# Performance work log

Measured on AMD Instinct MI355X. Metric: run time of the kernel, lower is better.

Reference implementation:

```python
import jax, jax.numpy as jnp
import numpy as np

B = 64        # number of tasks (sequential steps)
D = 512       # knowledge_representation_dim == understanding_representation_dim
M = 8192      # memory_slots
GAMMA = 0.95  # memory_gamma


def setup_inputs() -> dict:
    key = jax.random.key(0)
    k1, k2, k3, k4 = jax.random.split(key, 4)
    ortho = jax.nn.initializers.orthogonal()
    return {
        "k": jax.random.normal(k1, (B, 1, D), jnp.float32),
        "u": jax.random.normal(k2, (B, 1, D), jnp.float32),
        "memory_knowledge": ortho(k3, (D, M), jnp.float32),
        "memory_understanding": ortho(k4, (D, M), jnp.float32),
        "beta_param": jnp.float32(0.0),
        "memory_gamma": jnp.float32(GAMMA),
    }


def reference(k, u, memory_knowledge, memory_understanding, beta_param, memory_gamma):
    n_slots = memory_knowledge.shape[1]
    slot_ids = jnp.arange(n_slots)
    beta = jax.nn.sigmoid(beta_param)

    def step(carry, xs):
        MK, MU, w_w, w_u, w_lu = carry
        k_task, u_task = xs  # each [1, D]
        # cosine similarity of the task key against every memory column: [1, M]
        sim = (k_task @ MK) / (
            jnp.linalg.norm(k_task, axis=-1, keepdims=True)
            * jnp.linalg.norm(MK, axis=0, keepdims=True)
        )
        w_r = jax.nn.softmax(sim, axis=-1)[0]  # [M]
        # zero out the least-used slot (argmin of usage weights)
        keep = (slot_ids != jnp.argmin(w_u))[None, :]  # [1, M]
        MK = jnp.where(keep, MK, 0.0)
        MU = jnp.where(keep, MU, 0.0)
        # usage / write / least-used weight updates
        w_u = memory_gamma * w_u + w_r + w_w
        w_w = beta * jnp.mean(w_r) + (1.0 - beta) * w_lu  # [M] via broadcast of scalar mean
        w_lu = (slot_ids == jnp.argmin(w_u)).astype(MK.dtype)  # one-hot least-used
        # rank-1 write of understanding, then read refined understanding, then write knowledge
        MU = MU + u_task[0][:, None] * w_w[None, :]  # [D, M]
        u_ref = w_r @ MK.T  # [D] -- read uses MK after zeroing, before its write
        MK = MK + k_task[0][:, None] * w_w[None, :]  # [D, M]
        return (MK, MU, w_w, w_u, w_lu), u_ref

    zeros = jnp.zeros((n_slots,), memory_knowledge.dtype)
    init = (memory_knowledge, memory_understanding, zeros, zeros, zeros)
    _, u_refined = jax.lax.scan(step, init, (k, u))
    return u_refined[:, None, :]  # [B, 1, D]
```

## Files before the change

kernel.cpp:

```cpp
#include <hip/hip_runtime.h>
#include <math.h>

#define BB 64
#define DD 512
#define MM 8192
#define K2T 512
#define K2C 16

typedef unsigned long long u64;

template<int CTRL>
__device__ __forceinline__ float dpp_addf(float x) {
    int y = __builtin_amdgcn_update_dpp(0, __float_as_int(x), CTRL, 0xF, 0xF, true);
    return x + __int_as_float(y);
}
__device__ __forceinline__ float wave_sum64(float x) {
    x = dpp_addf<0x111>(x); x = dpp_addf<0x112>(x); x = dpp_addf<0x114>(x); x = dpp_addf<0x118>(x);
    x = dpp_addf<0x142>(x); x = dpp_addf<0x143>(x);
    return __int_as_float(__builtin_amdgcn_readlane(__float_as_int(x), 63));
}
template<int CTRL>
__device__ __forceinline__ u64 dpp_min_step(u64 k) {
    unsigned lo = (unsigned)k, hi = (unsigned)(k >> 32);
    unsigned nlo = (unsigned)__builtin_amdgcn_update_dpp((int)0xFFFFFFFFu, (int)lo, CTRL, 0xF, 0xF, false);
    unsigned nhi = (unsigned)__builtin_amdgcn_update_dpp((int)0xFFFFFFFFu, (int)hi, CTRL, 0xF, 0xF, false);
    u64 nk = (((u64)nhi) << 32) | (u64)nlo;
    return nk < k ? nk : k;
}
__device__ __forceinline__ u64 wave_min64(u64 k) {
    k = dpp_min_step<0x111>(k); k = dpp_min_step<0x112>(k); k = dpp_min_step<0x114>(k);
    k = dpp_min_step<0x118>(k); k = dpp_min_step<0x142>(k); k = dpp_min_step<0x143>(k);
    unsigned lo = (unsigned)__builtin_amdgcn_readlane((int)(unsigned)k, 63);
    unsigned hi = (unsigned)__builtin_amdgcn_readlane((int)(unsigned)(k >> 32), 63);
    return (((u64)hi) << 32) | (u64)lo;
}
__device__ __forceinline__ u64 wave_min8(u64 k) {
    k = dpp_min_step<0x111>(k); k = dpp_min_step<0x112>(k); k = dpp_min_step<0x114>(k);
    unsigned lo = (unsigned)__builtin_amdgcn_readlane((int)(unsigned)k, 7);
    unsigned hi = (unsigned)__builtin_amdgcn_readlane((int)(unsigned)(k >> 32), 7);
    return (((u64)hi) << 32) | (u64)lo;
}
__device__ __forceinline__ float readlane_f(float v, int l) {
    return __int_as_float(__builtin_amdgcn_readlane(__float_as_int(v), l));
}

__global__ __launch_bounds__(1024) void k0_gram(const float* __restrict__ K, float* __restrict__ G,
                                                float* __restrict__ Pfx) {
    __shared__ float Ks[BB][129];
    __shared__ float Gs[BB][BB];
    int tid = threadIdx.x;
    int s = tid & 63, tq = tid >> 6;
    float acc[4] = {0.f, 0.f, 0.f, 0.f};
    for (int d0 = 0; d0 < DD; d0 += 128) {
        #pragma unroll
        for (int i = 0; i < 8; ++i) {
            int e = i * 1024 + tid; int r = e >> 7, c = e & 127;
            Ks[r][c] = K[r * DD + d0 + c];
        }
        __syncthreads();
        for (int dl = 0; dl < 128; ++dl) {
            float kv = Ks[s][dl];
            #pragma unroll
            for (int i = 0; i < 4; ++i) acc[i] += Ks[tq * 4 + i][dl] * kv;
        }
        __syncthreads();
    }
    #pragma unroll
    for (int i = 0; i < 4; ++i) {
        G[(tq * 4 + i) * BB + s] = acc[i];
        Gs[tq * 4 + i][s] = acc[i];
    }
    __syncthreads();
    #pragma unroll
    for (int r = 0; r < 4; ++r) {
        int row = tq * 4 + r;
        float x = (s < row) ? Gs[row][s] : 0.f;
        #pragma unroll
        for (int o = 1; o < 64; o <<= 1) {
            float y = __shfl_down(x, o);
            if (s + o < 64) x += y;
        }
        Pfx[row * BB + s] = x;
    }
}

__global__ __launch_bounds__(256) void k1_s0(const float* __restrict__ K, const float* __restrict__ MK0,
                                             float* __restrict__ S0p, float* __restrict__ n2p) {
    __shared__ float Ks[64 * 65];
    __shared__ float Ms[64 * 65];
    __shared__ float sq[4 * 64];
    const int tid = threadIdx.x;
    const int lane = tid & 63, w = tid >> 6;
    const int jb = blockIdx.x * 64;
    const int dbase = blockIdx.y * 256;
    const int t4 = ((w << 2) | (lane >> 4)) << 2;
    const int jq0 = lane & 15;
    float acc[4][4];
    #pragma unroll
    for (int i = 0; i < 4; ++i)
        #pragma unroll
        for (int q = 0; q < 4; ++q) acc[i][q] = 0.f;
    float sqa = 0.f;
    for (int dt = 0; dt < 4; ++dt) {
        int d0 = dbase + dt * 64;
        #pragma unroll
        for (int i = 0; i < 16; ++i) {
            int e = i * 256 + tid; int r = e >> 6, c = e & 63;
            Ks[r * 65 + c] = K[r * DD + d0 + c];
            float m = MK0[(d0 + r) * MM + jb + c];
            Ms[r * 65 + c] = m;
            sqa += m * m;
        }
        __syncthreads();
        #pragma unroll 4
        for (int dl = 0; dl < 64; ++dl) {
            float kv[4], mv[4];
            #pragma unroll
            for (int i = 0; i < 4; ++i) kv[i] = Ks[(t4 + i) * 65 + dl];
            #pragma unroll
            for (int q = 0; q < 4; ++q) mv[q] = Ms[dl * 65 + jq0 + 16 * q];
            #pragma unroll
            for (int i = 0; i < 4; ++i)
                #pragma unroll
                for (int q = 0; q < 4; ++q) acc[i][q] += kv[i] * mv[q];
        }
        __syncthreads();
    }
    #pragma unroll
    for (int i = 0; i < 4; ++i)
        #pragma unroll
        for (int q = 0; q < 4; ++q)
            S0p[blockIdx.y * BB * MM + (t4 + i) * MM + jb + jq0 + 16 * q] = acc[i][q];
    sq[w * 64 + lane] = sqa;
    __syncthreads();
    if (w == 0) n2p[blockIdx.y * MM + jb + lane] =
        sq[lane] + sq[64 + lane] + sq[128 + lane] + sq[192 + lane];
}

__global__ __launch_bounds__(256) void k1b_ecold(const float* __restrict__ S0p,
                                                 const float* __restrict__ G,
                                                 const float* __restrict__ Pfx,
                                                 const float* __restrict__ n2p,
                                                 const float* __restrict__ bp,
                                                 float* __restrict__ Ecold) {
    __shared__ float Pfx0s[BB], invks[BB], k2s[BB];
    int tid = threadIdx.x;
    int j = blockIdx.x * 256 + tid;
    if (tid < BB) {
        float g = G[tid * BB + tid];
        k2s[tid] = g;
        invks[tid] = __builtin_amdgcn_rsqf(g);
        Pfx0s[tid] = Pfx[tid * BB + 0];
    }
    const float beta = 1.f / (1.f + expf(-bp[0]));
    const float cuni = beta / (float)MM;
    float n2c = n2p[j] + n2p[MM + j];
    __syncthreads();
    for (int t = 0; t < BB; ++t) {
        float s0 = S0p[t * MM + j] + S0p[(BB + t) * MM + j];
        float d_ = s0 + cuni * Pfx0s[t];
        float cosv = d_ * invks[t] * __builtin_amdgcn_rsqf(n2c);
        float ee = __expf(cosv);
        Ecold[t * MM + j] = ee;
        n2c = n2c + 2.f * cuni * d_ + cuni * cuni * k2s[t];
    }
}

__global__ __launch_bounds__(256) void ks_rowsum(const float* __restrict__ Ecold, float* __restrict__ Scold) {
    __shared__ float sw[4];
    int t = blockIdx.x, tid = threadIdx.x;
    int lane = tid & 63, wid = tid >> 6;
    float s = 0.f;
    #pragma unroll
    for (int i = 0; i < 32; ++i) s += Ecold[t * MM + i * 256 + tid];
    #pragma unroll
    for (int o = 32; o > 0; o >>= 1) s += __shfl_down(s, o);
    if (lane == 0) sw[wid] = s;
    __syncthreads();
    if (tid == 0) Scold[t] = sw[0] + sw[1] + sw[2] + sw[3];
}

struct ScanSmem {
    u64   red[2][8];
    float EtabL[BB * BB];
    float EcTabL[BB * BB];
    float invSL[BB];
    float SL[BB];
    int   endL[BB];
};
struct K3Smem {
    float Ws[64 * 65];
    float Msub[64 * 65];
};
#define SMEM_BYTES ((sizeof(ScanSmem) > sizeof(K3Smem)) ? sizeof(ScanSmem) : sizeof(K3Smem))

__global__ __launch_bounds__(512) void k23_scan_u1(const float* __restrict__ Ecold,
                                                   const float* __restrict__ G,
                                                   const float* __restrict__ Pfx,
                                                   const float* __restrict__ Scoldg,
                                                   const float* __restrict__ bp,
                                                   const float* __restrict__ gp,
                                                   const float* __restrict__ MK0,
                                                   float* __restrict__ Etab_g,
                                                   float* __restrict__ EcTab_g,
                                                   float* __restrict__ Sg,
                                                   float* __restrict__ invSg,
                                                   int*   __restrict__ endTab_g,
                                                   int*   __restrict__ hcolg,
                                                   float* __restrict__ parts) {
    __shared__ __align__(16) char smem_raw[SMEM_BYTES];
    const int tid = threadIdx.x;

    if (blockIdx.x != 0) {
        K3Smem* sm = (K3Smem*)smem_raw;
        const int tile = blockIdx.x - 1;
        const int d0 = (tile & 7) * 64;
        const int by = tile >> 3;
        const bool act = tid < 256;
        const int lane = tid & 63, w = tid >> 6;
        const int t4 = ((w << 2) | (lane >> 4)) << 2;
        const int dq0 = lane & 15;
        float acc[4][4];
        #pragma unroll
        for (int i = 0; i < 4; ++i)
            #pragma unroll
            for (int q = 0; q < 4; ++q) acc[i][q] = 0.f;
        for (int sub = 0; sub < 4; ++sub) {
            int jb = by * 256 + sub * 64;
            if (act) {
                #pragma unroll
                for (int i = 0; i < 16; ++i) {
                    int e = i * 256 + tid; int r = e >> 6, c = e & 63;
                    sm->Ws[r * 65 + c] = Ecold[r * MM + jb + c];
                    sm->Msub[r * 65 + c] = MK0[(d0 + r) * MM + jb + c];
                }
            }
            __syncthreads();
            if (act) {
                #pragma unroll 4
                for (int jl = 0; jl < 64; ++jl) {
                    float wv[4], mv[4];
                    #pragma unroll
                    for (int i = 0; i < 4; ++i) wv[i] = sm->Ws[(t4 + i) * 65 + jl];
                    #pragma unroll
                    for (int q = 0; q < 4; ++q) mv[q] = sm->Msub[(dq0 + 16 * q) * 65 + jl];
                    #pragma unroll
                    for (int i = 0; i < 4; ++i)
                        #pragma unroll
                        for (int q = 0; q < 4; ++q) acc[i][q] += wv[i] * mv[q];
                }
            }
            __syncthreads();
        }
        if (act) {
            #pragma unroll
            for (int i = 0; i < 4; ++i)
                #pragma unroll
                for (int q = 0; q < 4; ++q)
                    parts[(by * 64 + t4 + i) * DD + d0 + dq0 + 16 * q] = acc[i][q];
        }
        return;
    }

    ScanSmem* sm = (ScanSmem*)smem_raw;
    const int lane = tid & 63;
    const int wid = tid >> 6;

    const float beta  = 1.f / (1.f + expf(-bp[0]));
    const float gamma = gp[0];
    const float cuni  = beta / (float)MM;
    const float omb   = 1.f - beta;

    if (tid < BB) sm->endL[tid] = BB;

    const float4* Ec4 = reinterpret_cast<const float4*>(Ecold);

    float wu[K2C], eb0[K2C], eb1[K2C];
    #pragma unroll
    for (int c = 0; c < K2C; ++c) wu[c] = 0.f;
    #pragma unroll
    for (int i = 0; i < K2C / 4; ++i) {
        float4 v = Ec4[i * K2T + tid];
        eb0[4 * i + 0] = v.x; eb0[4 * i + 1] = v.y; eb0[4 * i + 2] = v.z; eb0[4 * i + 3] = v.w;
    }

    float slot_n2 = 0.f, slot_E = 0.f, slot_ec = 0.f, slot_ecpf = 0.f, wu_hot = 0.f;
    int   slot_j = -1;
    bool  slot_act = false;

    float grow_c = G[lane], pfx_c = Pfx[lane];
    float Ssc_c = Scoldg[0];
    __syncthreads();

    auto step = [&](int t, float (&cur)[K2C], float (&nxt)[K2C]) {
        int j0; float minval;
        if (t == 0) { j0 = 0; minval = 0.f; }
        else {
            u64 pm = sm->red[t & 1][lane & 7];
            pm = wave_min8(pm);
            j0 = (int)(pm & 0xFFFFFFFFu);
            minval = __uint_as_float((unsigned)(pm >> 32));
        }

        float latev = 0.f;
        if (lane == t) latev = Ecold[t * MM + j0];
        if (t + 1 < BB) {
            int js = (lane == t) ? j0 : slot_j;
            if (slot_act || lane == t) slot_ecpf = Ecold[(t + 1) * MM + js];
        }
        float grow_n = (t + 1 < BB) ? G[(t + 1) * BB + lane] : 0.f;
        float pfx_n  = (t + 1 < BB) ? Pfx[(t + 1) * BB + lane] : 0.f;
        float Ssc_n  = (t + 1 < BB) ? Scoldg[t + 1] : 0.f;
        __builtin_amdgcn_sched_barrier(0);
        if (t + 1 < BB) {
            #pragma unroll
            for (int i = 0; i < K2C / 4; ++i) {
                float4 v = Ec4[(t + 1) * (MM / 4) + i * K2T + tid];
                nxt[4 * i + 0] = v.x; nxt[4 * i + 1] = v.y; nxt[4 * i + 2] = v.z; nxt[4 * i + 3] = v.w;
            }
        }
        __builtin_amdgcn_sched_barrier(0);

        const float k2t  = readlane_f(grow_c, t);
        const float invk = __builtin_amdgcn_rsqf(k2t);

        u64 sup = __ballot(slot_act && (slot_j == j0));
        const bool has_sup = (sup != 0ull);
        const int  ssup = has_sup ? (int)__builtin_ctzll(sup) : 0;

        float myDelta = 0.f, e_true = 0.f;
        if (slot_act) {
            float d_ = cuni * pfx_c;
            if (lane >= 1) d_ += omb * grow_c;
            e_true = __expf(d_ * invk * __builtin_amdgcn_rsqf(slot_n2));
            myDelta = e_true - slot_ec;
            slot_E = e_true;
            slot_n2 = slot_n2 + 2.f * cuni * d_ + cuni * cuni * k2t;
        }

        const float S = Ssc_c + wave_sum64(myDelta);
        const float invS = __builtin_amdgcn_rcpf(S);
        const float cuni_t = (t == 0) ? 0.f : cuni;

        if (slot_act) {
            float ww = cuni + ((t >= 2 && lane == t - 1) ? omb : 0.f);
            wu_hot = fmaf(gamma, wu_hot, fmaf(e_true, invS, ww));
        }

        float trans_wu = readlane_f(wu_hot, ssup);
        float trans_E  = readlane_f(e_true, ssup);
        if (lane == t) {
            slot_j = j0;
            float ww0 = cuni + ((t >= 1) ? omb : 0.f);
            slot_n2 = ww0 * ww0 * k2t;
            slot_act = true;
            slot_ec = latev;
            float fresh_wu = fmaf(gamma, minval, fmaf(latev, invS, cuni_t));
            wu_hot = has_sup ? trans_wu : fresh_wu;
            slot_E = has_sup ? trans_E : latev;
        }
        if (has_sup) {
            if (lane == ssup) slot_act = false;
            if (wid == 0 && lane == t) sm->endL[ssup] = t;
        }

        float vmin = 0.f; int jmin = 0;
        #pragma unroll
        for (int i = 0; i < 4; ++i) {
            #pragma unroll
            for (int q = 0; q < 4; ++q) {
                int c = i * 4 + q;
                float wun = fmaf(gamma, wu[c], fmaf(cur[c], invS, cuni_t));
                wu[c] = wun;
                int j = i * 2048 + (tid << 2) + q;
                if (c == 0) { vmin = wun; jmin = j; }
                else if (wun < vmin) { vmin = wun; jmin = j; }
            }
        }
        u64 key = (((u64)__float_as_uint(vmin)) << 32) | (unsigned)jmin;

        if (((j0 >> 2) & (K2T - 1)) == tid) {
            int cj = ((j0 >> 11) << 2) | (j0 & 3);
            #pragma unroll
            for (int c = 0; c < K2C; ++c) if (c == cj) wu[c] = __builtin_inff();
        }

        u64 skey = slot_act ? ((((u64)__float_as_uint(wu_hot)) << 32) | (unsigned)slot_j) : ~0ull;
        key = skey < key ? skey : key;
        key = wave_min64(key);
        if (lane == 0) sm->red[(t + 1) & 1][wid] = key;

        if (wid == 0) {
            sm->EtabL[t * BB + lane]  = slot_E;
            sm->EcTabL[t * BB + lane] = slot_ec;
            if (lane == 0) { sm->invSL[t] = invS; sm->SL[t] = S; }
        }

        if (slot_act) slot_ec = slot_ecpf;
        grow_c = grow_n; pfx_c = pfx_n; Ssc_c = Ssc_n;

        asm volatile("s_waitcnt lgkmcnt(0)" ::: "memory");
        __builtin_amdgcn_s_barrier();
        asm volatile("" ::: "memory");
    };

    #pragma unroll 1
    for (int th = 0; th < BB; th += 2) {
        step(th, eb0, eb1);
        step(th + 1, eb1, eb0);
    }

    for (int i = tid; i < BB * BB; i += K2T) {
        Etab_g[i]  = sm->EtabL[i];
        EcTab_g[i] = sm->EcTabL[i];
    }
    if (tid < BB) {
        Sg[tid] = sm->SL[tid];
        invSg[tid] = sm->invSL[tid];
        endTab_g[tid] = sm->endL[tid];
    }
    if (wid == 0) hcolg[lane] = slot_j;
}

__global__ __launch_bounds__(512) void k3b_gather(const float* __restrict__ MK0, const int* __restrict__ hcolg,
                                                  float* __restrict__ MKhot) {
    int i = blockIdx.x, d = threadIdx.x;
    int h = hcolg[i];
    MKhot[i * DD + d] = MK0[d * MM + h];
}

__global__ __launch_bounds__(512) void k4_final(const float* __restrict__ parts,
                                                const float* __restrict__ K,
                                                const float* __restrict__ Etab,
                                                const float* __restrict__ EcTab,
                                                const int*   __restrict__ endTab,
                                                const float* __restrict__ Sg,
                                                const float* __restrict__ invSg,
                                                const float* __restrict__ MKhot,
                                                const float* __restrict__ bp,
                                                float* __restrict__ out) {
    __shared__ float Arow[BB];
    __shared__ float Drow[BB];
    int t = blockIdx.x, d = threadIdx.x;
    if (d < BB) {
        const float beta = 1.f / (1.f + expf(-bp[0]));
        const float cuni = beta / (float)MM;
        const float omb  = 1.f - beta;
        int s = d;
        float Ev = Etab[t * BB + s];
        int endv = endTab[s];
        bool act = (s <= t) && (t < endv);
        float S = Sg[t], invS = invSg[t];
        float ev = act ? Ev : 0.f;
        float x = ev;
        #pragma unroll
        for (int o = 1; o < 64; o <<= 1) {
            float y = __shfl_down(x, o);
            if (s + o < 64) x += y;
        }
        float suf = x - ev;
        float arow = 0.f;
        if (s < t) {
            float Qe = S - suf;
            arow = cuni * Qe;
            if (s >= 1 && act) arow += omb * Ev;
            arow *= invS;
        }
        Arow[s] = arow;
        Drow[s] = act ? (-invS * EcTab[t * BB + s]) : 0.f;
    }
    __syncthreads();
    float isv = invSg[t];
    float s1 = 0.f;
    #pragma unroll
    for (int p = 0; p < 32; ++p) s1 += parts[(p * 64 + t) * DD + d];
    float s2 = 0.f;
    for (int i = 0; i < BB; ++i) s2 += Drow[i] * MKhot[i * DD + d];
    float s3 = 0.f;
    for (int i = 0; i < BB; ++i) s3 += Arow[i] * K[i * DD + d];
    out[t * DD + d] = isv * s1 + s2 + s3;
}

extern "C" void kernel_launch(void* const* d_in, const int* in_sizes, int n_in,
                              void* d_out, int out_size, void* d_ws, size_t ws_size,
                              hipStream_t stream) {
    const float* K   = (const float*)d_in[0];
    const float* MK0 = (const float*)d_in[2];
    const float* bp  = (const float*)d_in[4];
    const float* gp  = (const float*)d_in[5];

    float* ws    = (float*)d_ws;
    float* G     = ws;
    float* Pfx   = G + 4096;
    float* S0p   = Pfx + 4096;
    float* n2p   = S0p + 1048576;
    float* Ecold = n2p + 16384;
    float* Scold = Ecold + 524288;
    float* Etab  = Scold + 64;
    float* EcTab = Etab + 4096;
    float* Sarr  = EcTab + 4096;
    float* invS  = Sarr + 64;
    float* MKhot = invS + 64;
    float* parts = MKhot + 32768;
    int*   hcol  = (int*)(parts + 1048576);
    int*   endT  = hcol + 64;
    float* out   = (float*)d_out;

    k0_gram     <<<1, 1024, 0, stream>>>(K, G, Pfx);
    k1_s0       <<<dim3(128, 2), 256, 0, stream>>>(K, MK0, S0p, n2p);
    k1b_ecold   <<<32, 256, 0, stream>>>(S0p, G, Pfx, n2p, bp, Ecold);
    ks_rowsum   <<<64, 256, 0, stream>>>(Ecold, Scold);
    k23_scan_u1 <<<257, 512, 0, stream>>>(Ecold, G, Pfx, Scold, bp, gp, MK0,
                                          Etab, EcTab, Sarr, invS, endT, hcol, parts);
    k3b_gather  <<<64, 512, 0, stream>>>(MK0, hcol, MKhot);
    k4_final    <<<64, 512, 0, stream>>>(parts, K, Etab, EcTab, endT, Sarr, invS, MKhot, bp, out);
}
```

Before: 253.6 us.

## Merge gram and S0 kernels; restrict scan slot logic to wave zero

Folds the single-block Gram/prefix kernel into the S0 GEMM kernel as an extra block 0, which removes one launch and lets the two run concurrently. In the sequential scan, the hot-slot bookkeeping now runs only on wave 0, and invS reaches the other waves through shared memory behind an added barrier. Fresh-slot initialisation moves after the key reduction, and the wave min reads lane 63 directly instead of using readlanes. This adds a second barrier per scan step, which may offset the savings on the serial critical path.

```diff
diff --git a/kernel.cpp b/kernel.cpp
--- a/kernel.cpp
+++ b/kernel.cpp
@@ -27,12 +27,10 @@
     u64 nk = (((u64)nhi) << 32) | (u64)nlo;
     return nk < k ? nk : k;
 }
-__device__ __forceinline__ u64 wave_min64(u64 k) {
+__device__ __forceinline__ u64 wave_min64_lane63(u64 k) {
     k = dpp_min_step<0x111>(k); k = dpp_min_step<0x112>(k); k = dpp_min_step<0x114>(k);
     k = dpp_min_step<0x118>(k); k = dpp_min_step<0x142>(k); k = dpp_min_step<0x143>(k);
-    unsigned lo = (unsigned)__builtin_amdgcn_readlane((int)(unsigned)k, 63);
-    unsigned hi = (unsigned)__builtin_amdgcn_readlane((int)(unsigned)(k >> 32), 63);
-    return (((u64)hi) << 32) | (u64)lo;
+    return k;
 }
 __device__ __forceinline__ u64 wave_min8(u64 k) {
     k = dpp_min_step<0x111>(k); k = dpp_min_step<0x112>(k); k = dpp_min_step<0x114>(k);
@@ -44,55 +42,80 @@
     return __int_as_float(__builtin_amdgcn_readlane(__float_as_int(v), l));
 }
 
-__global__ __launch_bounds__(1024) void k0_gram(const float* __restrict__ K, float* __restrict__ G,
-                                                float* __restrict__ Pfx) {
-    __shared__ float Ks[BB][129];
-    __shared__ float Gs[BB][BB];
-    int tid = threadIdx.x;
-    int s = tid & 63, tq = tid >> 6;
-    float acc[4] = {0.f, 0.f, 0.f, 0.f};
-    for (int d0 = 0; d0 < DD; d0 += 128) {
-        #pragma unroll
-        for (int i = 0; i < 8; ++i) {
-            int e = i * 1024 + tid; int r = e >> 7, c = e & 127;
-            Ks[r][c] = K[r * DD + d0 + c];
-        }
+struct K0Smem {
+    float Ks[BB][129];
+    float Gs[BB][BB];
+};
+struct K1Smem {
+    float Ks[64 * 65];
+    float Ms[64 * 65];
+    float sq[4 * 64];
+};
+#define KA_SMEM ((sizeof(K0Smem) > sizeof(K1Smem)) ? sizeof(K0Smem) : sizeof(K1Smem))
+
+__global__ __launch_bounds__(256) void ka_gram_s0(const float* __restrict__ K, const float* __restrict__ MK0,
+                                                  float* __restrict__ G, float* __restrict__ Pfx,
+                                                  float* __restrict__ S0p, float* __restrict__ n2p) {
+    __shared__ __align__(16) char blob[KA_SMEM];
+    const int tid = threadIdx.x;
+
+    if (blockIdx.x == 0) {
+        K0Smem* sm = (K0Smem*)blob;
+        const int ti = ((tid >> 4) & 15) << 2;
+        const int tj = (tid & 15) << 2;
+        float acc[4][4];
+        #pragma unroll
+        for (int i = 0; i < 4; ++i)
+            #pragma unroll
+            for (int j = 0; j < 4; ++j) acc[i][j] = 0.f;
+        for (int d0 = 0; d0 < DD; d0 += 128) {
+            #pragma unroll
+            for (int i = 0; i < 32; ++i) {
+                int e = i * 256 + tid; int r = e >> 7, c = e & 127;
+                sm->Ks[r][c] = K[r * DD + d0 + c];
+            }
+            __syncthreads();
+            for (int dl = 0; dl < 128; ++dl) {
+                float rv[4], cv[4];
+                #pragma unroll
+                for (int i = 0; i < 4; ++i) rv[i] = sm->Ks[ti + i][dl];
+                #pragma unroll
+                for (int j = 0; j < 4; ++j) cv[j] = sm->Ks[tj + j][dl];
+                #pragma unroll
+                for (int i = 0; i < 4; ++i)
+                    #pragma unroll
+                    for (int j = 0; j < 4; ++j) acc[i][j] += rv[i] * cv[j];
+            }
+            __syncthreads();
+        }
+        #pragma unroll
+        for (int i = 0; i < 4; ++i)
+            #pragma unroll
+            for (int j = 0; j < 4; ++j) {
+                G[(ti + i) * BB + tj + j] = acc[i][j];
+                sm->Gs[ti + i][tj + j] = acc[i][j];
+            }
         __syncthreads();
-        for (int dl = 0; dl < 128; ++dl) {
-            float kv = Ks[s][dl];
-            #pragma unroll
-            for (int i = 0; i < 4; ++i) acc[i] += Ks[tq * 4 + i][dl] * kv;
-        }
-        __syncthreads();
-    }
-    #pragma unroll
-    for (int i = 0; i < 4; ++i) {
-        G[(tq * 4 + i) * BB + s] = acc[i];
-        Gs[tq * 4 + i][s] = acc[i];
-    }
-    __syncthreads();
-    #pragma unroll
-    for (int r = 0; r < 4; ++r) {
-        int row = tq * 4 + r;
-        float x = (s < row) ? Gs[row][s] : 0.f;
-        #pragma unroll
-        for (int o = 1; o < 64; o <<= 1) {
-            float y = __shfl_down(x, o);
-            if (s + o < 64) x += y;
-        }
-        Pfx[row * BB + s] = x;
-    }
-}
-
-__global__ __launch_bounds__(256) void k1_s0(const float* __restrict__ K, const float* __restrict__ MK0,
-                                             float* __restrict__ S0p, float* __restrict__ n2p) {
-    __shared__ float Ks[64 * 65];
-    __shared__ float Ms[64 * 65];
-    __shared__ float sq[4 * 64];
-    const int tid = threadIdx.x;
+        const int s = tid & 63, w = tid >> 6;
+        for (int rr = 0; rr < 16; ++rr) {
+            int row = w * 16 + rr;
+            float x = (s < row) ? sm->Gs[row][s] : 0.f;
+            #pragma unroll
+            for (int o = 1; o < 64; o <<= 1) {
+                float y = __shfl_down(x, o);
+                if (s + o < 64) x += y;
+            }
+            Pfx[row * BB + s] = x;
+        }
+        return;
+    }
+
+    K1Smem* sm = (K1Smem*)blob;
+    const int b = blockIdx.x - 1;
     const int lane = tid & 63, w = tid >> 6;
-    const int jb = blockIdx.x * 64;
-    const int dbase = blockIdx.y * 256;
+    const int jb = (b & 127) * 64;
+    const int by = b >> 7;
+    const int dbase = by * 256;
     const int t4 = ((w << 2) | (lane >> 4)) << 2;
     const int jq0 = lane & 15;
     float acc[4][4];
@@ -106,9 +129,9 @@
         #pragma unroll
         for (int i = 0; i < 16; ++i) {
             int e = i * 256 + tid; int r = e >> 6, c = e & 63;
-            Ks[r * 65 + c] = K[r * DD + d0 + c];
+            sm->Ks[r * 65 + c] = K[r * DD + d0 + c];
             float m = MK0[(d0 + r) * MM + jb + c];
-            Ms[r * 65 + c] = m;
+            sm->Ms[r * 65 + c] = m;
             sqa += m * m;
         }
         __syncthreads();
@@ -116,9 +139,9 @@
         for (int dl = 0; dl < 64; ++dl) {
             float kv[4], mv[4];
             #pragma unroll
-            for (int i = 0; i < 4; ++i) kv[i] = Ks[(t4 + i) * 65 + dl];
-            #pragma unroll
-            for (int q = 0; q < 4; ++q) mv[q] = Ms[dl * 65 + jq0 + 16 * q];
+            for (int i = 0; i < 4; ++i) kv[i] = sm->Ks[(t4 + i) * 65 + dl];
+            #pragma unroll
+            for (int q = 0; q < 4; ++q) mv[q] = sm->Ms[dl * 65 + jq0 + 16 * q];
             #pragma unroll
             for (int i = 0; i < 4; ++i)
                 #pragma unroll
@@ -130,11 +153,11 @@
     for (int i = 0; i < 4; ++i)
         #pragma unroll
         for (int q = 0; q < 4; ++q)
-            S0p[blockIdx.y * BB * MM + (t4 + i) * MM + jb + jq0 + 16 * q] = acc[i][q];
-    sq[w * 64 + lane] = sqa;
+            S0p[by * BB * MM + (t4 + i) * MM + jb + jq0 + 16 * q] = acc[i][q];
+    sm->sq[w * 64 + lane] = sqa;
     __syncthreads();
-    if (w == 0) n2p[blockIdx.y * MM + jb + lane] =
-        sq[lane] + sq[64 + lane] + sq[128 + lane] + sq[192 + lane];
+    if (w == 0) n2p[by * MM + jb + lane] =
+        sm->sq[lane] + sm->sq[64 + lane] + sm->sq[128 + lane] + sm->sq[192 + lane];
 }
 
 __global__ __launch_bounds__(256) void k1b_ecold(const float* __restrict__ S0p,
@@ -187,6 +210,7 @@
     float invSL[BB];
     float SL[BB];
     int   endL[BB];
+    float invS_bc;
 };
 struct K3Smem {
     float Ws[64 * 65];
@@ -265,6 +289,7 @@
     ScanSmem* sm = (ScanSmem*)smem_raw;
     const int lane = tid & 63;
     const int wid = tid >> 6;
+    const bool w0 = (wid == 0);
 
     const float beta  = 1.f / (1.f + expf(-bp[0]));
     const float gamma = gp[0];
@@ -288,8 +313,8 @@
     int   slot_j = -1;
     bool  slot_act = false;
 
-    float grow_c = G[lane], pfx_c = Pfx[lane];
-    float Ssc_c = Scoldg[0];
+    float grow_c = 0.f, pfx_c = 0.f, Ssc_c = 0.f;
+    if (w0) { grow_c = G[lane]; pfx_c = Pfx[lane]; Ssc_c = Scoldg[0]; }
     __syncthreads();
 
     auto step = [&](int t, float (&cur)[K2C], float (&nxt)[K2C]) {
@@ -301,16 +326,20 @@
             j0 = (int)(pm & 0xFFFFFFFFu);
             minval = __uint_as_float((unsigned)(pm >> 32));
         }
+        const float cuni_t = (t == 0) ? 0.f : cuni;
 
         float latev = 0.f;
-        if (lane == t) latev = Ecold[t * MM + j0];
-        if (t + 1 < BB) {
+        if (w0 && lane == t) latev = Ecold[t * MM + j0];
+        if (w0 && t + 1 < BB) {
             int js = (lane == t) ? j0 : slot_j;
             if (slot_act || lane == t) slot_ecpf = Ecold[(t + 1) * MM + js];
         }
-        float grow_n = (t + 1 < BB) ? G[(t + 1) * BB + lane] : 0.f;
-        float pfx_n  = (t + 1 < BB) ? Pfx[(t + 1) * BB + lane] : 0.f;
-        float Ssc_n  = (t + 1 < BB) ? Scoldg[t + 1] : 0.f;
+        float grow_n = 0.f, pfx_n = 0.f, Ssc_n = 0.f;
+        if (w0 && t + 1 < BB) {
+            grow_n = G[(t + 1) * BB + lane];
+            pfx_n  = Pfx[(t + 1) * BB + lane];
+            Ssc_n  = Scoldg[t + 1];
+        }
         __builtin_amdgcn_sched_barrier(0);
         if (t + 1 < BB) {
             #pragma unroll
@@ -321,48 +350,55 @@
         }
         __builtin_amdgcn_sched_barrier(0);
 
-        const float k2t  = readlane_f(grow_c, t);
-        const float invk = __builtin_amdgcn_rsqf(k2t);
-
-        u64 sup = __ballot(slot_act && (slot_j == j0));
-        const bool has_sup = (sup != 0ull);
-        const int  ssup = has_sup ? (int)__builtin_ctzll(sup) : 0;
-
-        float myDelta = 0.f, e_true = 0.f;
-        if (slot_act) {
-            float d_ = cuni * pfx_c;
-            if (lane >= 1) d_ += omb * grow_c;
-            e_true = __expf(d_ * invk * __builtin_amdgcn_rsqf(slot_n2));
-            myDelta = e_true - slot_ec;
-            slot_E = e_true;
-            slot_n2 = slot_n2 + 2.f * cuni * d_ + cuni * cuni * k2t;
-        }
-
-        const float S = Ssc_c + wave_sum64(myDelta);
-        const float invS = __builtin_amdgcn_rcpf(S);
-        const float cuni_t = (t == 0) ? 0.f : cuni;
-
-        if (slot_act) {
-            float ww = cuni + ((t >= 2 && lane == t - 1) ? omb : 0.f);
-            wu_hot = fmaf(gamma, wu_hot, fmaf(e_true, invS, ww));
-        }
-
-        float trans_wu = readlane_f(wu_hot, ssup);
-        float trans_E  = readlane_f(e_true, ssup);
-        if (lane == t) {
-            slot_j = j0;
-            float ww0 = cuni + ((t >= 1) ? omb : 0.f);
-            slot_n2 = ww0 * ww0 * k2t;
-            slot_act = true;
-            slot_ec = latev;
-            float fresh_wu = fmaf(gamma, minval, fmaf(latev, invS, cuni_t));
-            wu_hot = has_sup ? trans_wu : fresh_wu;
-            slot_E = has_sup ? trans_E : latev;
-        }
-        if (has_sup) {
-            if (lane == ssup) slot_act = false;
-            if (wid == 0 && lane == t) sm->endL[ssup] = t;
-        }
+        float invS = 0.f, S = 0.f, e_true = 0.f;
+        bool fresh = false;
+        if (w0) {
+            const float k2t  = readlane_f(grow_c, t);
+            const float invk = __builtin_amdgcn_rsqf(k2t);
+
+            u64 sup = __ballot(slot_act && (slot_j == j0));
+            const bool has_sup = (sup != 0ull);
+            const int  ssup = has_sup ? (int)__builtin_ctzll(sup) : 0;
+
+            float myDelta = 0.f;
+            if (slot_act) {
+                float d_ = cuni * pfx_c;
+                if (lane >= 1) d_ += omb * grow_c;
+                e_true = __expf(d_ * invk * __builtin_amdgcn_rsqf(slot_n2));
+                myDelta = e_true - slot_ec;
+                slot_E = e_true;
+                slot_n2 = slot_n2 + 2.f * cuni * d_ + cuni * cuni * k2t;
+            }
+
+            S = Ssc_c + wave_sum64(myDelta);
+            invS = __builtin_amdgcn_rcpf(S);
+            sm->invS_bc = invS;
+
+            if (slot_act) {
+                float ww = cuni + ((t >= 2 && lane == t - 1) ? omb : 0.f);
+                wu_hot = fmaf(gamma, wu_hot, fmaf(e_true, invS, ww));
+            }
+
+            float trans_wu = readlane_f(wu_hot, ssup);
+            float trans_E  = readlane_f(e_true, ssup);
+            if (lane == t) {
+                slot_j = j0;
+                float ww0 = cuni + ((t >= 1) ? omb : 0.f);
+                slot_n2 = ww0 * ww0 * k2t;
+                slot_act = true;
+                if (has_sup) { wu_hot = trans_wu; slot_E = trans_E; }
+                fresh = !has_sup;
+            }
+            if (has_sup) {
+                if (lane == ssup) slot_act = false;
+                if (lane == t) sm->endL[ssup] = t;
+            }
+        }
+
+        asm volatile("s_waitcnt lgkmcnt(0)" ::: "memory");
+        __builtin_amdgcn_s_barrier();
+        asm volatile("" ::: "memory");
+        if (!w0) invS = sm->invS_bc;
 
         float vmin = 0.f; int jmin = 0;
         #pragma unroll
@@ -385,19 +421,26 @@
             for (int c = 0; c < K2C; ++c) if (c == cj) wu[c] = __builtin_inff();
         }
 
-        u64 skey = slot_act ? ((((u64)__float_as_uint(wu_hot)) << 32) | (unsigned)slot_j) : ~0ull;
-        key = skey < key ? skey : key;
-        key = wave_min64(key);
-        if (lane == 0) sm->red[(t + 1) & 1][wid] = key;
-
-        if (wid == 0) {
+        if (w0) {
+            u64 skey = (slot_act && !fresh)
+                     ? ((((u64)__float_as_uint(wu_hot)) << 32) | (unsigned)slot_j) : ~0ull;
+            key = skey < key ? skey : key;
+        }
+        key = wave_min64_lane63(key);
+        if (lane == 63) sm->red[(t + 1) & 1][wid] = key;
+
+        if (w0) {
+            if (lane == t) slot_ec = latev;
+            if (fresh) {
+                slot_E  = latev;
+                wu_hot  = fmaf(gamma, minval, fmaf(latev, invS, cuni_t));
+            }
             sm->EtabL[t * BB + lane]  = slot_E;
             sm->EcTabL[t * BB + lane] = slot_ec;
             if (lane == 0) { sm->invSL[t] = invS; sm->SL[t] = S; }
-        }
-
-        if (slot_act) slot_ec = slot_ecpf;
-        grow_c = grow_n; pfx_c = pfx_n; Ssc_c = Ssc_n;
+            if (slot_act) slot_ec = slot_ecpf;
+            grow_c = grow_n; pfx_c = pfx_n; Ssc_c = Ssc_n;
+        }
 
         asm volatile("s_waitcnt lgkmcnt(0)" ::: "memory");
         __builtin_amdgcn_s_barrier();
@@ -419,7 +462,7 @@
         invSg[tid] = sm->invSL[tid];
         endTab_g[tid] = sm->endL[tid];
     }
-    if (wid == 0) hcolg[lane] = slot_j;
+    if (w0) hcolg[lane] = slot_j;
 }
 
 __global__ __launch_bounds__(512) void k3b_gather(const float* __restrict__ MK0, const int* __restrict__ hcolg,
@@ -506,8 +549,7 @@
     int*   endT  = hcol + 64;
     float* out   = (float*)d_out;
 
-    k0_gram     <<<1, 1024, 0, stream>>>(K, G, Pfx);
-    k1_s0       <<<dim3(128, 2), 256, 0, stream>>>(K, MK0, S0p, n2p);
+    ka_gram_s0  <<<257, 256, 0, stream>>>(K, MK0, G, Pfx, S0p, n2p);
     k1b_ecold   <<<32, 256, 0, stream>>>(S0p, G, Pfx, n2p, bp, Ecold);
     ks_rowsum   <<<64, 256, 0, stream>>>(Ecold, Scold);
     k23_scan_u1 <<<257, 512, 0, stream>>>(Ecold, G, Pfx, Scold, bp, gp, MK0,
```

Measured after the change: 220.8 us. 12.9% less time.

## Fuse S0 GEMM, cold-exp and row-sum kernels into scan pipeline

Applied to the files above, without the earlier changes.

Merges k1_s0 and k1b_ecold into one kernel that keeps the full-depth dot products in shared memory and computes the cold exponentials directly. This drops the split-D partials and their global round trip. The separate row-sum kernel is removed; the serial scan kernel now computes each row sum itself from a triple-buffered prefetch two steps ahead, with only wave 0 doing the hot-slot bookkeeping and broadcasting invS through LDS. It cuts two launches and global traffic, but halves the S0 grid parallelism (128 blocks instead of 256) and adds an extra barrier per scan step.

```diff
diff --git a/kernel.cpp b/kernel.cpp
--- a/kernel.cpp
+++ b/kernel.cpp
@@ -18,6 +18,13 @@
     x = dpp_addf<0x111>(x); x = dpp_addf<0x112>(x); x = dpp_addf<0x114>(x); x = dpp_addf<0x118>(x);
     x = dpp_addf<0x142>(x); x = dpp_addf<0x143>(x);
     return __int_as_float(__builtin_amdgcn_readlane(__float_as_int(x), 63));
+}
+__device__ __forceinline__ float readlane_f(float v, int l) {
+    return __int_as_float(__builtin_amdgcn_readlane(__float_as_int(v), l));
+}
+__device__ __forceinline__ float wave_sum8(float x) {
+    x = dpp_addf<0x111>(x); x = dpp_addf<0x112>(x); x = dpp_addf<0x114>(x);
+    return readlane_f(x, 7);
 }
 template<int CTRL>
 __device__ __forceinline__ u64 dpp_min_step(u64 k) {
@@ -27,21 +34,16 @@
     u64 nk = (((u64)nhi) << 32) | (u64)nlo;
     return nk < k ? nk : k;
 }
-__device__ __forceinline__ u64 wave_min64(u64 k) {
+__device__ __forceinline__ u64 wave_min64_lane63(u64 k) {
     k = dpp_min_step<0x111>(k); k = dpp_min_step<0x112>(k); k = dpp_min_step<0x114>(k);
     k = dpp_min_step<0x118>(k); k = dpp_min_step<0x142>(k); k = dpp_min_step<0x143>(k);
-    unsigned lo = (unsigned)__builtin_amdgcn_readlane((int)(unsigned)k, 63);
-    unsigned hi = (unsigned)__builtin_amdgcn_readlane((int)(unsigned)(k >> 32), 63);
-    return (((u64)hi) << 32) | (u64)lo;
+    return k;
 }
 __device__ __forceinline__ u64 wave_min8(u64 k) {
     k = dpp_min_step<0x111>(k); k = dpp_min_step<0x112>(k); k = dpp_min_step<0x114>(k);
     unsigned lo = (unsigned)__builtin_amdgcn_readlane((int)(unsigned)k, 7);
     unsigned hi = (unsigned)__builtin_amdgcn_readlane((int)(unsigned)(k >> 32), 7);
     return (((u64)hi) << 32) | (u64)lo;
-}
-__device__ __forceinline__ float readlane_f(float v, int l) {
-    return __int_as_float(__builtin_amdgcn_readlane(__float_as_int(v), l));
 }
 
 __global__ __launch_bounds__(1024) void k0_gram(const float* __restrict__ K, float* __restrict__ G,
@@ -84,32 +86,43 @@
     }
 }
 
-__global__ __launch_bounds__(256) void k1_s0(const float* __restrict__ K, const float* __restrict__ MK0,
-                                             float* __restrict__ S0p, float* __restrict__ n2p) {
+__global__ __launch_bounds__(256) void kb_ecold(const float* __restrict__ K, const float* __restrict__ MK0,
+                                                const float* __restrict__ G, const float* __restrict__ Pfx,
+                                                const float* __restrict__ bp,
+                                                float* __restrict__ Ecold) {
     __shared__ float Ks[64 * 65];
     __shared__ float Ms[64 * 65];
+    __shared__ float S0s[64 * 65];
     __shared__ float sq[4 * 64];
+    __shared__ float n2A[64];
+    __shared__ float n2full[64];
+    __shared__ float Pfx0s[BB], invks[BB], k2s[BB];
     const int tid = threadIdx.x;
     const int lane = tid & 63, w = tid >> 6;
     const int jb = blockIdx.x * 64;
-    const int dbase = blockIdx.y * 256;
     const int t4 = ((w << 2) | (lane >> 4)) << 2;
     const int jq0 = lane & 15;
-    float acc[4][4];
+    if (tid < BB) {
+        float g = G[tid * BB + tid];
+        k2s[tid] = g;
+        invks[tid] = __builtin_amdgcn_rsqf(g);
+        Pfx0s[tid] = Pfx[tid * BB + 0];
+    }
+    float accA[4][4], accB[4][4];
     #pragma unroll
     for (int i = 0; i < 4; ++i)
         #pragma unroll
-        for (int q = 0; q < 4; ++q) acc[i][q] = 0.f;
-    float sqa = 0.f;
+        for (int q = 0; q < 4; ++q) { accA[i][q] = 0.f; accB[i][q] = 0.f; }
+    float sqaA = 0.f, sqaB = 0.f;
     for (int dt = 0; dt < 4; ++dt) {
-        int d0 = dbase + dt * 64;
+        int d0 = dt * 64;
         #pragma unroll
         for (int i = 0; i < 16; ++i) {
             int e = i * 256 + tid; int r = e >> 6, c = e & 63;
             Ks[r * 65 + c] = K[r * DD + d0 + c];
             float m = MK0[(d0 + r) * MM + jb + c];
             Ms[r * 65 + c] = m;
-            sqa += m * m;
+            sqaA += m * m;
         }
         __syncthreads();
         #pragma unroll 4
@@ -122,71 +135,76 @@
             #pragma unroll
             for (int i = 0; i < 4; ++i)
                 #pragma unroll
-                for (int q = 0; q < 4; ++q) acc[i][q] += kv[i] * mv[q];
+                for (int q = 0; q < 4; ++q) accA[i][q] += kv[i] * mv[q];
         }
         __syncthreads();
     }
+    for (int dt = 0; dt < 4; ++dt) {
+        int d0 = 256 + dt * 64;
+        #pragma unroll
+        for (int i = 0; i < 16; ++i) {
+            int e = i * 256 + tid; int r = e >> 6, c = e & 63;
+            Ks[r * 65 + c] = K[r * DD + d0 + c];
+            float m = MK0[(d0 + r) * MM + jb + c];
+            Ms[r * 65 + c] = m;
+            sqaB += m * m;
+        }
+        __syncthreads();
+        #pragma unroll 4
+        for (int dl = 0; dl < 64; ++dl) {
+            float kv[4], mv[4];
+            #pragma unroll
+            for (int i = 0; i < 4; ++i) kv[i] = Ks[(t4 + i) * 65 + dl];
+            #pragma unroll
+            for (int q = 0; q < 4; ++q) mv[q] = Ms[dl * 65 + jq0 + 16 * q];
+            #pragma unroll
+            for (int i = 0; i < 4; ++i)
+                #pragma unroll
+                for (int q = 0; q < 4; ++q) accB[i][q] += kv[i] * mv[q];
+        }
+        __syncthreads();
+    }
+    sq[w * 64 + lane] = sqaA;
+    __syncthreads();
+    if (w == 0) n2A[lane] = sq[lane] + sq[64 + lane] + sq[128 + lane] + sq[192 + lane];
+    __syncthreads();
+    sq[w * 64 + lane] = sqaB;
+    __syncthreads();
+    if (w == 0) {
+        float b4 = sq[lane] + sq[64 + lane] + sq[128 + lane] + sq[192 + lane];
+        n2full[lane] = n2A[lane] + b4;
+    }
     #pragma unroll
     for (int i = 0; i < 4; ++i)
         #pragma unroll
         for (int q = 0; q < 4; ++q)
-            S0p[blockIdx.y * BB * MM + (t4 + i) * MM + jb + jq0 + 16 * q] = acc[i][q];
-    sq[w * 64 + lane] = sqa;
-    __syncthreads();
-    if (w == 0) n2p[blockIdx.y * MM + jb + lane] =
-        sq[lane] + sq[64 + lane] + sq[128 + lane] + sq[192 + lane];
-}
-
-__global__ __launch_bounds__(256) void k1b_ecold(const float* __restrict__ S0p,
-                                                 const float* __restrict__ G,
-                                                 const float* __restrict__ Pfx,
-                                                 const float* __restrict__ n2p,
-                                                 const float* __restrict__ bp,
-                                                 float* __restrict__ Ecold) {
-    __shared__ float Pfx0s[BB], invks[BB], k2s[BB];
-    int tid = threadIdx.x;
-    int j = blockIdx.x * 256 + tid;
-    if (tid < BB) {
-        float g = G[tid * BB + tid];
-        k2s[tid] = g;
-        invks[tid] = __builtin_amdgcn_rsqf(g);
-        Pfx0s[tid] = Pfx[tid * BB + 0];
-    }
-    const float beta = 1.f / (1.f + expf(-bp[0]));
-    const float cuni = beta / (float)MM;
-    float n2c = n2p[j] + n2p[MM + j];
-    __syncthreads();
-    for (int t = 0; t < BB; ++t) {
-        float s0 = S0p[t * MM + j] + S0p[(BB + t) * MM + j];
-        float d_ = s0 + cuni * Pfx0s[t];
-        float cosv = d_ * invks[t] * __builtin_amdgcn_rsqf(n2c);
-        float ee = __expf(cosv);
-        Ecold[t * MM + j] = ee;
-        n2c = n2c + 2.f * cuni * d_ + cuni * cuni * k2s[t];
-    }
-}
-
-__global__ __launch_bounds__(256) void ks_rowsum(const float* __restrict__ Ecold, float* __restrict__ Scold) {
-    __shared__ float sw[4];
-    int t = blockIdx.x, tid = threadIdx.x;
-    int lane = tid & 63, wid = tid >> 6;
-    float s = 0.f;
-    #pragma unroll
-    for (int i = 0; i < 32; ++i) s += Ecold[t * MM + i * 256 + tid];
-    #pragma unroll
-    for (int o = 32; o > 0; o >>= 1) s += __shfl_down(s, o);
-    if (lane == 0) sw[wid] = s;
-    __syncthreads();
-    if (tid == 0) Scold[t] = sw[0] + sw[1] + sw[2] + sw[3];
+            S0s[(t4 + i) * 65 + jq0 + 16 * q] = accA[i][q] + accB[i][q];
+    __syncthreads();
+    if (w == 0) {
+        const float beta = 1.f / (1.f + expf(-bp[0]));
+        const float cuni = beta / (float)MM;
+        int j = jb + lane;
+        float n2c = n2full[lane];
+        for (int t = 0; t < BB; ++t) {
+            float s0 = S0s[t * 65 + lane];
+            float d_ = s0 + cuni * Pfx0s[t];
+            float cosv = d_ * invks[t] * __builtin_amdgcn_rsqf(n2c);
+            float ee = __expf(cosv);
+            Ecold[t * MM + j] = ee;
+            n2c = n2c + 2.f * cuni * d_ + cuni * cuni * k2s[t];
+        }
+    }
 }
 
 struct ScanSmem {
     u64   red[2][8];
+    float rsum[2][8];
     float EtabL[BB * BB];
     float EcTabL[BB * BB];
     float invSL[BB];
     float SL[BB];
     int   endL[BB];
+    float invS_bc;
 };
 struct K3Smem {
     float Ws[64 * 65];
@@ -197,7 +215,6 @@
 __global__ __launch_bounds__(512) void k23_scan_u1(const float* __restrict__ Ecold,
                                                    const float* __restrict__ G,
                                                    const float* __restrict__ Pfx,
-                                                   const float* __restrict__ Scoldg,
                                                    const float* __restrict__ bp,
                                                    const float* __restrict__ gp,
                                                    const float* __restrict__ MK0,
@@ -265,6 +282,7 @@
     ScanSmem* sm = (ScanSmem*)smem_raw;
     const int lane = tid & 63;
     const int wid = tid >> 6;
+    const bool w0 = (wid == 0);
 
     const float beta  = 1.f / (1.f + expf(-bp[0]));
     const float gamma = gp[0];
@@ -275,24 +293,35 @@
 
     const float4* Ec4 = reinterpret_cast<const float4*>(Ecold);
 
-    float wu[K2C], eb0[K2C], eb1[K2C];
+    float wu[K2C], e0[K2C], e1[K2C], e2[K2C];
     #pragma unroll
     for (int c = 0; c < K2C; ++c) wu[c] = 0.f;
     #pragma unroll
     for (int i = 0; i < K2C / 4; ++i) {
         float4 v = Ec4[i * K2T + tid];
-        eb0[4 * i + 0] = v.x; eb0[4 * i + 1] = v.y; eb0[4 * i + 2] = v.z; eb0[4 * i + 3] = v.w;
+        e0[4 * i + 0] = v.x; e0[4 * i + 1] = v.y; e0[4 * i + 2] = v.z; e0[4 * i + 3] = v.w;
+        float4 u = Ec4[(MM / 4) + i * K2T + tid];
+        e1[4 * i + 0] = u.x; e1[4 * i + 1] = u.y; e1[4 * i + 2] = u.z; e1[4 * i + 3] = u.w;
+    }
+    {
+        float rs = e0[0];
+        #pragma unroll
+        for (int c = 1; c < K2C; ++c) rs += e0[c];
+        rs = wave_sum64(rs);
+        if (lane == 0) sm->rsum[0][wid] = rs;
     }
 
     float slot_n2 = 0.f, slot_E = 0.f, slot_ec = 0.f, slot_ecpf = 0.f, wu_hot = 0.f;
     int   slot_j = -1;
     bool  slot_act = false;
 
-    float grow_c = G[lane], pfx_c = Pfx[lane];
-    float Ssc_c = Scoldg[0];
-    __syncthreads();
-
-    auto step = [&](int t, float (&cur)[K2C], float (&nxt)[K2C]) {
+    float grow_c = 0.f, pfx_c = 0.f;
+    if (w0) { grow_c = G[lane]; pfx_c = Pfx[lane]; }
+    __syncthreads();
+
+    auto step = [&](int t, float (&cur)[K2C], float (&nx1)[K2C], float (&ld)[K2C]) {
+        float Ssc = 0.f;
+        if (w0) Ssc = wave_sum8(sm->rsum[t & 1][lane & 7]);
         int j0; float minval;
         if (t == 0) { j0 = 0; minval = 0.f; }
         else {
@@ -301,68 +330,78 @@
             j0 = (int)(pm & 0xFFFFFFFFu);
             minval = __uint_as_float((unsigned)(pm >> 32));
         }
+        const float cuni_t = (t == 0) ? 0.f : cuni;
 
         float latev = 0.f;
-        if (lane == t) latev = Ecold[t * MM + j0];
-        if (t + 1 < BB) {
+        if (w0 && lane == t) latev = Ecold[t * MM + j0];
+        if (w0 && t + 1 < BB) {
             int js = (lane == t) ? j0 : slot_j;
             if (slot_act || lane == t) slot_ecpf = Ecold[(t + 1) * MM + js];
         }
-        float grow_n = (t + 1 < BB) ? G[(t + 1) * BB + lane] : 0.f;
-        float pfx_n  = (t + 1 < BB) ? Pfx[(t + 1) * BB + lane] : 0.f;
-        float Ssc_n  = (t + 1 < BB) ? Scoldg[t + 1] : 0.f;
+        float grow_n = 0.f, pfx_n = 0.f;
+        if (w0 && t + 1 < BB) {
+            grow_n = G[(t + 1) * BB + lane];
+            pfx_n  = Pfx[(t + 1) * BB + lane];
+        }
         __builtin_amdgcn_sched_barrier(0);
-        if (t + 1 < BB) {
+        if (t + 2 < BB) {
             #pragma unroll
             for (int i = 0; i < K2C / 4; ++i) {
-                float4 v = Ec4[(t + 1) * (MM / 4) + i * K2T + tid];
-                nxt[4 * i + 0] = v.x; nxt[4 * i + 1] = v.y; nxt[4 * i + 2] = v.z; nxt[4 * i + 3] = v.w;
+                float4 v = Ec4[(t + 2) * (MM / 4) + i * K2T + tid];
+                ld[4 * i + 0] = v.x; ld[4 * i + 1] = v.y; ld[4 * i + 2] = v.z; ld[4 * i + 3] = v.w;
             }
         }
         __builtin_amdgcn_sched_barrier(0);
 
-        const float k2t  = readlane_f(grow_c, t);
-        const float invk = __builtin_amdgcn_rsqf(k2t);
-
-        u64 sup = __ballot(slot_act && (slot_j == j0));
-        const bool has_sup = (sup != 0ull);
-        const int  ssup = has_sup ? (int)__builtin_ctzll(sup) : 0;
-
-        float myDelta = 0.f, e_true = 0.f;
-        if (slot_act) {
-            float d_ = cuni * pfx_c;
-            if (lane >= 1) d_ += omb * grow_c;
-            e_true = __expf(d_ * invk * __builtin_amdgcn_rsqf(slot_n2));
-            myDelta = e_true - slot_ec;
-            slot_E = e_true;
-            slot_n2 = slot_n2 + 2.f * cuni * d_ + cuni * cuni * k2t;
-        }
-
-        const float S = Ssc_c + wave_sum64(myDelta);
-        const float invS = __builtin_amdgcn_rcpf(S);
-        const float cuni_t = (t == 0) ? 0.f : cuni;
-
-        if (slot_act) {
-            float ww = cuni + ((t >= 2 && lane == t - 1) ? omb : 0.f);
-            wu_hot = fmaf(gamma, wu_hot, fmaf(e_true, invS, ww));
-        }
-
-        float trans_wu = readlane_f(wu_hot, ssup);
-        float trans_E  = readlane_f(e_true, ssup);
-        if (lane == t) {
-            slot_j = j0;
-            float ww0 = cuni + ((t >= 1) ? omb : 0.f);
-            slot_n2 = ww0 * ww0 * k2t;
-            slot_act = true;
-            slot_ec = latev;
-            float fresh_wu = fmaf(gamma, minval, fmaf(latev, invS, cuni_t));
-            wu_hot = has_sup ? trans_wu : fresh_wu;
-            slot_E = has_sup ? trans_E : latev;
-        }
-        if (has_sup) {
-            if (lane == ssup) slot_act = false;
-            if (wid == 0 && lane == t) sm->endL[ssup] = t;
-        }
+        float invS = 0.f, S = 0.f, e_true = 0.f;
+        bool fresh = false;
+        if (w0) {
+            const float k2t  = readlane_f(grow_c, t);
+            const float invk = __builtin_amdgcn_rsqf(k2t);
+
+            u64 sup = __ballot(slot_act && (slot_j == j0));
+            const bool has_sup = (sup != 0ull);
+            const int  ssup = has_sup ? (int)__builtin_ctzll(sup) : 0;
+
+            float myDelta = 0.f;
+            if (slot_act) {
+                float d_ = cuni * pfx_c;
+                if (lane >= 1) d_ += omb * grow_c;
+                e_true = __expf(d_ * invk * __builtin_amdgcn_rsqf(slot_n2));
+                myDelta = e_true - slot_ec;
+                slot_E = e_true;
+                slot_n2 = slot_n2 + 2.f * cuni * d_ + cuni * cuni * k2t;
+            }
+
+            S = Ssc + wave_sum64(myDelta);
+            invS = __builtin_amdgcn_rcpf(S);
+            sm->invS_bc = invS;
+
+            if (slot_act) {
+                float ww = cuni + ((t >= 2 && lane == t - 1) ? omb : 0.f);
+                wu_hot = fmaf(gamma, wu_hot, fmaf(e_true, invS, ww));
+            }
+
+            float trans_wu = readlane_f(wu_hot, ssup);
+            float trans_E  = readlane_f(e_true, ssup);
+            if (lane == t) {
+                slot_j = j0;
+                float ww0 = cuni + ((t >= 1) ? omb : 0.f);
+                slot_n2 = ww0 * ww0 * k2t;
+                slot_act = true;
+                if (has_sup) { wu_hot = trans_wu; slot_E = trans_E; }
+                fresh = !has_sup;
+            }
+            if (has_sup) {
+                if (lane == ssup) slot_act = false;
+                if (lane == t) sm->endL[ssup] = t;
+            }
+        }
+
+        asm volatile("s_waitcnt lgkmcnt(0)" ::: "memory");
+        __builtin_amdgcn_s_barrier();
+        asm volatile("" ::: "memory");
+        if (!w0) invS = sm->invS_bc;
 
         float vmin = 0.f; int jmin = 0;
         #pragma unroll
@@ -385,19 +424,34 @@
             for (int c = 0; c < K2C; ++c) if (c == cj) wu[c] = __builtin_inff();
         }
 
-        u64 skey = slot_act ? ((((u64)__float_as_uint(wu_hot)) << 32) | (unsigned)slot_j) : ~0ull;
-        key = skey < key ? skey : key;
-        key = wave_min64(key);
-        if (lane == 0) sm->red[(t + 1) & 1][wid] = key;
-
-        if (wid == 0) {
+        if (t + 1 < BB) {
+            float rs = nx1[0];
+            #pragma unroll
+            for (int c = 1; c < K2C; ++c) rs += nx1[c];
+            rs = wave_sum64(rs);
+            if (lane == 0) sm->rsum[(t + 1) & 1][wid] = rs;
+        }
+
+        if (w0) {
+            u64 skey = (slot_act && !fresh)
+                     ? ((((u64)__float_as_uint(wu_hot)) << 32) | (unsigned)slot_j) : ~0ull;
+            key = skey < key ? skey : key;
+        }
+        key = wave_min64_lane63(key);
+        if (lane == 63) sm->red[(t + 1) & 1][wid] = key;
+
+        if (w0) {
+            if (lane == t) slot_ec = latev;
+            if (fresh) {
+                slot_E  = latev;
+                wu_hot  = fmaf(gamma, minval, fmaf(latev, invS, cuni_t));
+            }
             sm->EtabL[t * BB + lane]  = slot_E;
             sm->EcTabL[t * BB + lane] = slot_ec;
             if (lane == 0) { sm->invSL[t] = invS; sm->SL[t] = S; }
-        }
-
-        if (slot_act) slot_ec = slot_ecpf;
-        grow_c = grow_n; pfx_c = pfx_n; Ssc_c = Ssc_n;
+            if (slot_act) slot_ec = slot_ecpf;
+            grow_c = grow_n; pfx_c = pfx_n;
+        }
 
         asm volatile("s_waitcnt lgkmcnt(0)" ::: "memory");
         __builtin_amdgcn_s_barrier();
@@ -405,10 +459,12 @@
     };
 
     #pragma unroll 1
-    for (int th = 0; th < BB; th += 2) {
-        step(th, eb0, eb1);
-        step(th + 1, eb1, eb0);
-    }
+    for (int th = 0; th < 63; th += 3) {
+        step(th + 0, e0, e1, e2);
+        step(th + 1, e1, e2, e0);
+        step(th + 2, e2, e0, e1);
+    }
+    step(63, e0, e1, e2);
 
     for (int i = tid; i < BB * BB; i += K2T) {
         Etab_g[i]  = sm->EtabL[i];
@@ -419,7 +475,7 @@
         invSg[tid] = sm->invSL[tid];
         endTab_g[tid] = sm->endL[tid];
     }
-    if (wid == 0) hcolg[lane] = slot_j;
+    if (w0) hcolg[lane] = slot_j;
 }
 
 __global__ __launch_bounds__(512) void k3b_gather(const float* __restrict__ MK0, const int* __restrict__ hcolg,
@@ -492,11 +548,8 @@
     float* ws    = (float*)d_ws;
     float* G     = ws;
     float* Pfx   = G + 4096;
-    float* S0p   = Pfx + 4096;
-    float* n2p   = S0p + 1048576;
-    float* Ecold = n2p + 16384;
-    float* Scold = Ecold + 524288;
-    float* Etab  = Scold + 64;
+    float* Ecold = Pfx + 4096;
+    float* Etab  = Ecold + 524288;
     float* EcTab = Etab + 4096;
     float* Sarr  = EcTab + 4096;
     float* invS  = Sarr + 64;
@@ -507,10 +560,8 @@
     float* out   = (float*)d_out;
 
     k0_gram     <<<1, 1024, 0, stream>>>(K, G, Pfx);
-    k1_s0       <<<dim3(128, 2), 256, 0, stream>>>(K, MK0, S0p, n2p);
-    k1b_ecold   <<<32, 256, 0, stream>>>(S0p, G, Pfx, n2p, bp, Ecold);
-    ks_rowsum   <<<64, 256, 0, stream>>>(Ecold, Scold);
-    k23_scan_u1 <<<257, 512, 0, stream>>>(Ecold, G, Pfx, Scold, bp, gp, MK0,
+    kb_ecold    <<<128, 256, 0, stream>>>(K, MK0, G, Pfx, bp, Ecold);
+    k23_scan_u1 <<<257, 512, 0, stream>>>(Ecold, G, Pfx, bp, gp, MK0,
                                           Etab, EcTab, Sarr, invS, endT, hcol, parts);
     k3b_gather  <<<64, 512, 0, stream>>>(MK0, hcol, MKhot);
     k4_final    <<<64, 512, 0, stream>>>(parts, K, Etab, EcTab, endT, Sarr, invS, MKhot, bp, out);
```

After: 258.2 us. Within noise of the previous version (+1.8%).
